# Kernel optimization log

Measured on AMD Instinct MI355X. Metric: run time of the kernel, lower is better.

The kernel has to match this reference:

```python
import jax, jax.numpy as jnp
import numpy as np

PIXEL_SIZE = 0.1
PI = 3.141592653589793


def setup_inputs() -> dict:
    key = jax.random.key(0)
    batch = jax.random.normal(key, (128, 1, 512, 512), dtype=jnp.float32)
    return {"batch": batch}


def _hann_window(roi):
    # lin = linspace(-roi/2, roi/2, roi); r[i,j] = sqrt(lin[j]^2 + lin[i]^2)
    lin = jnp.linspace(-roi / 2, roi / 2, roi, dtype=jnp.float32)
    r = jnp.sqrt(lin[None, :] ** 2 + lin[:, None] ** 2)
    hann = 0.5 * (1.0 + jnp.cos(PI * r / (roi / 2)))
    hann = jnp.where(r > roi / 2, 0.0, hann)
    return hann  # [roi, roi]


def _radial_segments(roi, n_freq):
    # radialDst = round(sqrt(xx^2 + yy^2)) with x = arange(-cx, roi-cx)
    cx = roi // 2
    x = np.arange(-cx, roi - cx, dtype=np.float64)
    xx, yy = np.meshgrid(x, x, indexing="ij")
    rad = np.round(np.sqrt(xx ** 2 + yy ** 2)).astype(np.int32)
    # bins >= n_freq go into an overflow segment that is discarded
    seg = np.where(rad < n_freq, rad, n_freq)
    return jnp.asarray(seg.ravel())


def reference(batch):
    px = PIXEL_SIZE
    roi = batch.shape[-1]
    cx = roi // 2
    n_freq = cx + 1
    nyquist = 1.0 / (2.0 * px)

    # subtract per-ROI mean
    batch_nm = batch - jnp.mean(batch, axis=(2, 3), keepdims=True)

    # Hann-windowed 2D power spectrum, averaged over realizations
    hann = _hann_window(roi)[None, None, :, :]
    F = jnp.fft.fftshift(jnp.fft.fft2(batch_nm * hann, axes=(2, 3)), axes=(2, 3))
    ps = jnp.mean(jnp.abs(F) ** 2, axis=0)            # [1, roi, roi]
    nps2D = (px ** 2 / roi ** 2) * jnp.squeeze(ps)    # [roi, roi]

    # single-pass radial mean binning (replaces per-k boolean-mask loop)
    seg = _radial_segments(roi, n_freq)
    flat = nps2D.ravel()
    sums = jax.ops.segment_sum(flat, seg, num_segments=n_freq + 1)[:n_freq]
    counts = jax.ops.segment_sum(jnp.ones_like(flat), seg, num_segments=n_freq + 1)[:n_freq]
    nps1D = sums / counts

    f1D = jnp.linspace(0.0, nyquist, n_freq, dtype=jnp.float32)
    return nps1D, nps2D, f1D
```

## Files before the change

kernel.cpp:

```cpp
#include <hip/hip_runtime.h>
#include <hip/hip_fp16.h>

#define N 512
#define NF 257
#define NB 128
#define PI_F 3.14159265358979323846f
#define C_SQ2 0.70710678118654752440f

__device__ __forceinline__ float2 cmul(float2 a, float2 b) {
    return make_float2(a.x * b.x - a.y * b.y, a.x * b.y + a.y * b.x);
}
__device__ __forceinline__ void bf(float2& a, float2& b) {
    float2 t = b;
    b = make_float2(a.x - t.x, a.y - t.y);
    a = make_float2(a.x + t.x, a.y + t.y);
}
__device__ __forceinline__ void bf_tw(float2& a, float2& b, float2 w) {
    float2 t = cmul(b, w);
    b = make_float2(a.x - t.x, a.y - t.y);
    a = make_float2(a.x + t.x, a.y + t.y);
}
__device__ __forceinline__ void bf_ni(float2& a, float2& b) {
    float2 t = make_float2(b.y, -b.x);
    b = make_float2(a.x - t.x, a.y - t.y);
    a = make_float2(a.x + t.x, a.y + t.y);
}
__device__ __forceinline__ void lds_order() {
    asm volatile("" ::: "memory");
}

__device__ __forceinline__ void fft_phaseA(float2 v[8]) {
    const float2 w64  = make_float2(C_SQ2, -C_SQ2);
    const float2 w192 = make_float2(-C_SQ2, -C_SQ2);
    bf(v[0], v[1]); bf(v[2], v[3]); bf(v[4], v[5]); bf(v[6], v[7]);
    bf(v[0], v[2]); bf_ni(v[1], v[3]); bf(v[4], v[6]); bf_ni(v[5], v[7]);
    bf(v[0], v[4]); bf_tw(v[1], v[5], w64); bf_ni(v[2], v[6]); bf_tw(v[3], v[7], w192);
}
__device__ __forceinline__ void fft_phaseBC(float2 v[8], float2 W1, float2 W1a,
                                            float2 W1n, float2 W1c, float2 W2,
                                            float2 W2n, float2 W3) {
    bf_tw(v[0], v[1], W3); bf_tw(v[2], v[3], W3); bf_tw(v[4], v[5], W3); bf_tw(v[6], v[7], W3);
    bf_tw(v[0], v[2], W2); bf_tw(v[1], v[3], W2n); bf_tw(v[4], v[6], W2); bf_tw(v[5], v[7], W2n);
    bf_tw(v[0], v[4], W1); bf_tw(v[1], v[5], W1a); bf_tw(v[2], v[6], W1n); bf_tw(v[3], v[7], W1c);
}

__device__ __forceinline__ void fft512_core(float2 v[8], float2* st, int l) {
    const float2 w64  = make_float2(C_SQ2, -C_SQ2);
    const float2 w192 = make_float2(-C_SQ2, -C_SQ2);
    int g = l >> 3, r = l & 7;
    lds_order();
    fft_phaseA(v);
#pragma unroll
    for (int e = 0; e < 8; e++) st[9 * l + e] = v[e];
    lds_order();
#pragma unroll
    for (int t = 0; t < 8; t++) v[t] = st[72 * g + 9 * t + r];
    float sn, cs;
    __sincosf(-(PI_F / 32.0f) * (float)r, &sn, &cs);
    float2 W1 = make_float2(cs, sn);
    float2 W2 = cmul(W1, W1);
    float2 W3 = cmul(W2, W2);
    float2 W2n = make_float2(W2.y, -W2.x);
    float2 W1a = cmul(W1, w64);
    float2 W1n = make_float2(W1.y, -W1.x);
    float2 W1c = cmul(W1, w192);
    fft_phaseBC(v, W1, W1a, W1n, W1c, W2, W2n, W3);
    lds_order();
#pragma unroll
    for (int t = 0; t < 8; t++) st[72 * g + 9 * t + r] = v[t];
    lds_order();
#pragma unroll
    for (int t = 0; t < 8; t++) v[t] = st[72 * t + l + (l >> 3)];
    __sincosf(-(PI_F / 256.0f) * (float)l, &sn, &cs);
    float2 Wc = make_float2(cs, sn);
    float2 w2 = cmul(Wc, Wc);
    float2 w4 = cmul(w2, w2);
    float2 w2n = make_float2(w2.y, -w2.x);
    float2 Wca = cmul(Wc, w64);
    float2 Wcn = make_float2(Wc.y, -Wc.x);
    float2 Wcc = cmul(Wc, w192);
    fft_phaseBC(v, Wc, Wca, Wcn, Wcc, w2, w2n, w4);
}

__device__ __forceinline__ void fft512_x2(float2 va[8], float2 vb[8], float2* st, int l) {
    const float2 w64  = make_float2(C_SQ2, -C_SQ2);
    const float2 w192 = make_float2(-C_SQ2, -C_SQ2);
    int g = l >> 3, r = l & 7;
    fft_phaseA(va); fft_phaseA(vb);
    lds_order();
#pragma unroll
    for (int e = 0; e < 8; e++) st[9 * l + e] = va[e];
    lds_order();
#pragma unroll
    for (int t = 0; t < 8; t++) va[t] = st[72 * g + 9 * t + r];
    lds_order();
#pragma unroll
    for (int e = 0; e < 8; e++) st[9 * l + e] = vb[e];
    lds_order();
#pragma unroll
    for (int t = 0; t < 8; t++) vb[t] = st[72 * g + 9 * t + r];
    float sn, cs;
    __sincosf(-(PI_F / 32.0f) * (float)r, &sn, &cs);
    float2 W1 = make_float2(cs, sn);
    float2 W2 = cmul(W1, W1);
    float2 W3 = cmul(W2, W2);
    float2 W2n = make_float2(W2.y, -W2.x);
    float2 W1a = cmul(W1, w64);
    float2 W1n = make_float2(W1.y, -W1.x);
    float2 W1c = cmul(W1, w192);
    fft_phaseBC(va, W1, W1a, W1n, W1c, W2, W2n, W3);
    fft_phaseBC(vb, W1, W1a, W1n, W1c, W2, W2n, W3);
    lds_order();
#pragma unroll
    for (int t = 0; t < 8; t++) st[72 * g + 9 * t + r] = va[t];
    lds_order();
#pragma unroll
    for (int t = 0; t < 8; t++) va[t] = st[72 * t + l + (l >> 3)];
    lds_order();
#pragma unroll
    for (int t = 0; t < 8; t++) st[72 * g + 9 * t + r] = vb[t];
    lds_order();
#pragma unroll
    for (int t = 0; t < 8; t++) vb[t] = st[72 * t + l + (l >> 3)];
    __sincosf(-(PI_F / 256.0f) * (float)l, &sn, &cs);
    float2 Wc = make_float2(cs, sn);
    float2 w2 = cmul(Wc, Wc);
    float2 w4 = cmul(w2, w2);
    float2 w2n = make_float2(w2.y, -w2.x);
    float2 Wca = cmul(Wc, w64);
    float2 Wcn = make_float2(Wc.y, -Wc.x);
    float2 Wcc = cmul(Wc, w192);
    fft_phaseBC(va, Wc, Wca, Wcn, Wcc, w2, w2n, w4);
    fft_phaseBC(vb, Wc, Wca, Wcn, Wcc, w2, w2n, w4);
}

__device__ __forceinline__ void unpack_rows(const float2 v[8], __half2* tile,
                                            int lr0, int lr1, int l, int sl) {
#pragma unroll
    for (int t = 0; t <= 4; t++) {
        float2 a = v[7 - t];
        float zfx = __shfl(a.x, sl);
        float zfy = __shfl(a.y, sl);
        if (l == 0) { float2 o = v[(8 - t) & 7]; zfx = o.x; zfy = o.y; }
        float2 z = v[t];
        int col = 64 * t + l;
        if (col < NF) {
            tile[lr0 * 265 + col] = __floats2half2_rn(0.5f * (z.x + zfx), 0.5f * (z.y - zfy));
            tile[lr1 * 265 + col] = __floats2half2_rn(0.5f * (z.y + zfy), 0.5f * (zfx - z.x));
        }
    }
}

__global__ void zero_kernel(float* __restrict__ accH, float* __restrict__ bins,
                            float* __restrict__ meanacc) {
    int i = blockIdx.x * blockDim.x + threadIdx.x;
    if (i < NF * N) accH[i] = 0.0f;
    if (i < 2 * (NF + 1)) bins[i] = 0.0f;
    if (i < NB) meanacc[i] = 0.0f;
}

__global__ __launch_bounds__(256) void hanntab_kernel(float* __restrict__ htab) {
    int i = blockIdx.x * 256 + threadIdx.x;
    int r = i >> 9, c = i & (N - 1);
    const float step = (float)N / (float)(N - 1);
    float a = -0.5f * (float)N + (float)r * step;
    float b = -0.5f * (float)N + (float)c * step;
    float rr = sqrtf(a * a + b * b);
    float h = (rr > 256.0f) ? 0.0f : 0.5f * (1.0f + cosf(rr * (PI_F / 256.0f)));
    htab[i] = h;
}

__global__ __launch_bounds__(512) void hannfft_kernel(const float* __restrict__ htab,
                                                      float2* __restrict__ Hrow) {
    __shared__ float sm[9216];
    int tid = threadIdx.x;
    int w = tid >> 6, l = tid & 63;
    int rowbase = blockIdx.x << 4;
    int r1 = rowbase + 2 * w;
    int rl = __brev((unsigned)l) >> 26;
    const int bre[8] = {0, 4, 2, 6, 1, 5, 3, 7};
    const float* h1 = htab + (size_t)r1 * N + rl;
    const float* h2 = h1 + N;

    float2 v[8];
#pragma unroll
    for (int e = 0; e < 8; e++) {
        int o = bre[e] << 6;
        v[e] = make_float2(h1[o], h2[o]);
    }

    float2* st = (float2*)sm + w * 576;
    fft512_core(v, st, l);
    __syncthreads();

    float* tre = sm;
    float* tim = sm + 4240;
    int lr0 = 2 * w, lr1 = lr0 + 1;
    int sl = (64 - l) & 63;
#pragma unroll
    for (int t = 0; t <= 4; t++) {
        float2 a = v[7 - t];
        float zfx = __shfl(a.x, sl);
        float zfy = __shfl(a.y, sl);
        if (l == 0) { float2 o = v[(8 - t) & 7]; zfx = o.x; zfy = o.y; }
        float2 z = v[t];
        int col = 64 * t + l;
        if (col < NF) {
            tre[lr0 * 265 + col] = 0.5f * (z.x + zfx);
            tim[lr0 * 265 + col] = 0.5f * (z.y - zfy);
            tre[lr1 * 265 + col] = 0.5f * (z.y + zfy);
            tim[lr1 * 265 + col] = 0.5f * (zfx - z.x);
        }
    }
    __syncthreads();

    int c0 = tid >> 4, rr = tid & 15;
#pragma unroll
    for (int it = 0; it < 9; it++) {
        int c = it * 32 + c0;
        if (c < NF) {
            float2 val = make_float2(tre[rr * 265 + c], tim[rr * 265 + c]);
            Hrow[(size_t)c * N + rowbase + rr] = val;
        }
    }
}

__global__ __launch_bounds__(512, 4) void rowfft_kernel(const float* __restrict__ x,
                                                        const float* __restrict__ htab,
                                                        float* __restrict__ meanacc,
                                                        __half2* __restrict__ inter) {
    __shared__ float sm[9216];
    __shared__ float redsum[8];
    int tid = threadIdx.x;
    int w = tid >> 6, l = tid & 63;
    int img = blockIdx.x >> 4;
    int rowbase = (blockIdx.x & 15) << 5;
    int r1 = rowbase + 4 * w;
    int rl = __brev((unsigned)l) >> 26;
    const int bre[8] = {0, 4, 2, 6, 1, 5, 3, 7};
    const float* xp = x + ((size_t)img * N + r1) * N + rl;
    const float* hp = htab + (size_t)r1 * N + rl;

    float ax[4][8], hx[4][8];
#pragma unroll
    for (int j = 0; j < 4; j++)
#pragma unroll
        for (int e = 0; e < 8; e++) ax[j][e] = xp[j * N + (bre[e] << 6)];
#pragma unroll
    for (int j = 0; j < 4; j++)
#pragma unroll
        for (int e = 0; e < 8; e++) hx[j][e] = hp[j * N + (bre[e] << 6)];
    __builtin_amdgcn_sched_barrier(0);

    float rsum = 0.0f;
#pragma unroll
    for (int j = 0; j < 4; j++)
#pragma unroll
        for (int e = 0; e < 8; e++) rsum += ax[j][e];

    float2 va[8], vb[8];
#pragma unroll
    for (int e = 0; e < 8; e++) {
        va[e] = make_float2(ax[0][e] * hx[0][e], ax[1][e] * hx[1][e]);
        vb[e] = make_float2(ax[2][e] * hx[2][e], ax[3][e] * hx[3][e]);
    }

#pragma unroll
    for (int off = 32; off > 0; off >>= 1) rsum += __shfl_down(rsum, off);
    if (l == 0) redsum[w] = rsum;

    float2* st = (float2*)sm + w * 576;
    fft512_x2(va, vb, st, l);
    __syncthreads();
    if (tid == 0) {
        float s = 0.0f;
#pragma unroll
        for (int i = 0; i < 8; i++) s += redsum[i];
        atomicAdd(meanacc + img, s);
    }

    __half2* tile = (__half2*)sm;
    int sl = (64 - l) & 63;
    unpack_rows(va, tile, 4 * w, 4 * w + 1, l, sl);
    unpack_rows(vb, tile, 4 * w + 2, 4 * w + 3, l, sl);
    __syncthreads();

    int c0 = tid >> 5, rr = tid & 31;
#pragma unroll
    for (int it = 0; it < 17; it++) {
        int c = it * 16 + c0;
        if (c < NF) {
            inter[((size_t)img * NF + c) * N + rowbase + rr] = tile[rr * 265 + c];
        }
    }
}

__global__ __launch_bounds__(256, 4) void colfft_kernel(const __half2* __restrict__ inter,
                                                        const float2* __restrict__ Hrow,
                                                        const float* __restrict__ meanacc,
                                                        float* __restrict__ accH) {
    __shared__ float sm[4608];
    int tid = threadIdx.x;
    int w = tid >> 6, l = tid & 63;
    int col = blockIdx.x * 4 + w;
    int colc = col < NF ? col : NF - 1;
    int b0 = blockIdx.y * 4;
    float2* st = (float2*)sm + w * 576;
    int rl = __brev((unsigned)l) >> 26;
    const int bre[8] = {0, 4, 2, 6, 1, 5, 3, 7};

    float2 hc[8];
    const float2* hp = Hrow + (size_t)colc * N + rl;
#pragma unroll
    for (int e = 0; e < 8; e++) hc[e] = hp[bre[e] << 6];

    float mn[4];
#pragma unroll
    for (int i = 0; i < 4; i++)
        mn[i] = meanacc[b0 + i] * (1.0f / ((float)N * (float)N));

    float pw[8];
#pragma unroll
    for (int t = 0; t < 8; t++) pw[t] = 0.0f;

    const size_t istr = (size_t)NF * N;
    const __half2* base = inter + ((size_t)b0 * NF + colc) * N + rl;

    __half2 cA[8], cB[8], nA[8], nB[8];
#pragma unroll
    for (int e = 0; e < 8; e++) {
        cA[e] = base[bre[e] << 6];
        cB[e] = base[istr + (bre[e] << 6)];
    }
    __builtin_amdgcn_sched_barrier(0);

#pragma unroll
    for (int it = 0; it < 2; it++) {
        if (it == 0) {
#pragma unroll
            for (int e = 0; e < 8; e++) {
                nA[e] = base[2 * istr + (bre[e] << 6)];
                nB[e] = base[3 * istr + (bre[e] << 6)];
            }
        }
        float mA = mn[2 * it], mB = mn[2 * it + 1];
        float2 va[8], vb[8];
#pragma unroll
        for (int e = 0; e < 8; e++) {
            float2 zA = __half22float2(cA[e]);
            float2 zB = __half22float2(cB[e]);
            va[e] = make_float2(zA.x - mA * hc[e].x, zA.y - mA * hc[e].y);
            vb[e] = make_float2(zB.x - mB * hc[e].x, zB.y - mB * hc[e].y);
        }
        fft512_x2(va, vb, st, l);
#pragma unroll
        for (int t = 0; t < 8; t++)
            pw[t] += va[t].x * va[t].x + va[t].y * va[t].y
                   + vb[t].x * vb[t].x + vb[t].y * vb[t].y;
#pragma unroll
        for (int e = 0; e < 8; e++) { cA[e] = nA[e]; cB[e] = nB[e]; }
    }

    if (col < NF) {
#pragma unroll
        for (int t = 0; t < 8; t++)
            atomicAdd(&accH[(size_t)col * N + 64 * t + l], pw[t]);
    }
}

__global__ __launch_bounds__(256) void finalize2d_kernel(const float* __restrict__ accH,
                                                         float* __restrict__ out2d,
                                                         float* __restrict__ bins) {
    __shared__ float lsum[NF];
    __shared__ float lcnt[NF];
    int t = threadIdx.x;
    for (int i = t; i < NF; i += 256) { lsum[i] = 0.0f; lcnt[i] = 0.0f; }
    __syncthreads();
    const float scale = (0.1f * 0.1f) / ((float)N * (float)N) / (float)NB;
    int idx = blockIdx.x * 256 + t;
    int stride = gridDim.x * 256;
    for (int p = idx; p < N * N; p += stride) {
        int i = p >> 9, j = p & (N - 1);
        int jm = (j + 256) & 511;
        int col, k;
        if (jm < NF) { col = jm; k = (i + 256) & 511; }
        else         { col = 256 - j; k = (256 - i) & 511; }
        float v = accH[((size_t)col << 9) + k] * scale;
        out2d[p] = v;
        float xi = (float)(i - 256), yj = (float)(j - 256);
        int rad = (int)rintf(sqrtf(xi * xi + yj * yj));
        if (rad < NF) { atomicAdd(&lsum[rad], v); atomicAdd(&lcnt[rad], 1.0f); }
    }
    __syncthreads();
    for (int i = t; i < NF; i += 256) {
        if (lsum[i] != 0.0f || lcnt[i] != 0.0f) {
            atomicAdd(&bins[i], lsum[i]);
            atomicAdd(&bins[NF + 1 + i], lcnt[i]);
        }
    }
}

__global__ void finalize1d_kernel(const float* __restrict__ bins, float* __restrict__ out) {
    int t = blockIdx.x * blockDim.x + threadIdx.x;
    if (t < NF) {
        out[t] = bins[t] / bins[NF + 1 + t];
        out[NF + N * N + t] = (float)t * (5.0f / 256.0f);
    }
}

extern "C" void kernel_launch(void* const* d_in, const int* in_sizes, int n_in,
                              void* d_out, int out_size, void* d_ws, size_t ws_size,
                              hipStream_t stream) {
    const float* x = (const float*)d_in[0];
    float* out = (float*)d_out;
    char* ws = (char*)d_ws;

    float* accH    = (float*)ws;
    float* meanacc = (float*)(ws + (size_t)NF * N * sizeof(float));
    float* bins    = meanacc + NB;
    size_t off_h = (size_t)NF * N * sizeof(float) + NB * sizeof(float)
                   + 2 * (NF + 1) * sizeof(float);
    off_h = (off_h + 255) & ~(size_t)255;
    float2* Hrow = (float2*)(ws + off_h);
    size_t off_t = off_h + (size_t)NF * N * sizeof(float2);
    off_t = (off_t + 255) & ~(size_t)255;
    float* htab = (float*)(ws + off_t);
    size_t off_inter = off_t + (size_t)N * N * sizeof(float);
    off_inter = (off_inter + 255) & ~(size_t)255;
    __half2* inter = (__half2*)(ws + off_inter);

    zero_kernel<<<dim3((NF * N + 255) / 256), dim3(256), 0, stream>>>(accH, bins, meanacc);
    hanntab_kernel<<<dim3(N * N / 256), dim3(256), 0, stream>>>(htab);
    hannfft_kernel<<<dim3(32), dim3(512), 0, stream>>>(htab, Hrow);
    rowfft_kernel<<<dim3(NB * 16), dim3(512), 0, stream>>>(x, htab, meanacc, inter);
    colfft_kernel<<<dim3(65, 32), dim3(256), 0, stream>>>(inter, Hrow, meanacc, accH);
    finalize2d_kernel<<<dim3(256), dim3(256), 0, stream>>>(accH, out + NF, bins);
    finalize1d_kernel<<<dim3(2), dim3(256), 0, stream>>>(bins, out);
}
```

Baseline: 256.1 us.

## Fold Hann-FFT and zeroing into other kernels and shrink row-FFT blocks

Merges the zero kernel into the Hann-table kernel and moves the Hann-window row FFT into extra blocks of the row-FFT kernel, which removes two launches. The row-FFT blocks shrink from 512 to 256 threads (16 rows per block, 8 blocks per CU hint) and twice as many blocks are launched. The sched_barrier is dropped and finalize2d gets more blocks. The Hann blocks now write Hrow directly with strided stores instead of staging through LDS, and they share the grid with the image row-FFT blocks.

Result: slower. 295.9 us (+15.5%).

```diff
diff --git a/kernel.cpp b/kernel.cpp
--- a/kernel.cpp
+++ b/kernel.cpp
@@ -42,44 +42,6 @@
     bf_tw(v[0], v[1], W3); bf_tw(v[2], v[3], W3); bf_tw(v[4], v[5], W3); bf_tw(v[6], v[7], W3);
     bf_tw(v[0], v[2], W2); bf_tw(v[1], v[3], W2n); bf_tw(v[4], v[6], W2); bf_tw(v[5], v[7], W2n);
     bf_tw(v[0], v[4], W1); bf_tw(v[1], v[5], W1a); bf_tw(v[2], v[6], W1n); bf_tw(v[3], v[7], W1c);
-}
-
-__device__ __forceinline__ void fft512_core(float2 v[8], float2* st, int l) {
-    const float2 w64  = make_float2(C_SQ2, -C_SQ2);
-    const float2 w192 = make_float2(-C_SQ2, -C_SQ2);
-    int g = l >> 3, r = l & 7;
-    lds_order();
-    fft_phaseA(v);
-#pragma unroll
-    for (int e = 0; e < 8; e++) st[9 * l + e] = v[e];
-    lds_order();
-#pragma unroll
-    for (int t = 0; t < 8; t++) v[t] = st[72 * g + 9 * t + r];
-    float sn, cs;
-    __sincosf(-(PI_F / 32.0f) * (float)r, &sn, &cs);
-    float2 W1 = make_float2(cs, sn);
-    float2 W2 = cmul(W1, W1);
-    float2 W3 = cmul(W2, W2);
-    float2 W2n = make_float2(W2.y, -W2.x);
-    float2 W1a = cmul(W1, w64);
-    float2 W1n = make_float2(W1.y, -W1.x);
-    float2 W1c = cmul(W1, w192);
-    fft_phaseBC(v, W1, W1a, W1n, W1c, W2, W2n, W3);
-    lds_order();
-#pragma unroll
-    for (int t = 0; t < 8; t++) st[72 * g + 9 * t + r] = v[t];
-    lds_order();
-#pragma unroll
-    for (int t = 0; t < 8; t++) v[t] = st[72 * t + l + (l >> 3)];
-    __sincosf(-(PI_F / 256.0f) * (float)l, &sn, &cs);
-    float2 Wc = make_float2(cs, sn);
-    float2 w2 = cmul(Wc, Wc);
-    float2 w4 = cmul(w2, w2);
-    float2 w2n = make_float2(w2.y, -w2.x);
-    float2 Wca = cmul(Wc, w64);
-    float2 Wcn = make_float2(Wc.y, -Wc.x);
-    float2 Wcc = cmul(Wc, w192);
-    fft_phaseBC(v, Wc, Wca, Wcn, Wcc, w2, w2n, w4);
 }
 
 __device__ __forceinline__ void fft512_x2(float2 va[8], float2 vb[8], float2* st, int l) {
@@ -151,15 +113,27 @@
     }
 }
 
-__global__ void zero_kernel(float* __restrict__ accH, float* __restrict__ bins,
-                            float* __restrict__ meanacc) {
-    int i = blockIdx.x * blockDim.x + threadIdx.x;
-    if (i < NF * N) accH[i] = 0.0f;
-    if (i < 2 * (NF + 1)) bins[i] = 0.0f;
-    if (i < NB) meanacc[i] = 0.0f;
-}
-
-__global__ __launch_bounds__(256) void hanntab_kernel(float* __restrict__ htab) {
+__device__ __forceinline__ void unpack_rows_store(const float2 v[8], float2* __restrict__ Hrow,
+                                                  int r0, int r1, int l, int sl) {
+#pragma unroll
+    for (int t = 0; t <= 4; t++) {
+        float2 a = v[7 - t];
+        float zfx = __shfl(a.x, sl);
+        float zfy = __shfl(a.y, sl);
+        if (l == 0) { float2 o = v[(8 - t) & 7]; zfx = o.x; zfy = o.y; }
+        float2 z = v[t];
+        int col = 64 * t + l;
+        if (col < NF) {
+            Hrow[(size_t)col * N + r0] = make_float2(0.5f * (z.x + zfx), 0.5f * (z.y - zfy));
+            Hrow[(size_t)col * N + r1] = make_float2(0.5f * (z.y + zfy), 0.5f * (zfx - z.x));
+        }
+    }
+}
+
+__global__ __launch_bounds__(256) void hanntab_zero_kernel(float* __restrict__ htab,
+                                                           float* __restrict__ accH,
+                                                           float* __restrict__ bins,
+                                                           float* __restrict__ meanacc) {
     int i = blockIdx.x * 256 + threadIdx.x;
     int r = i >> 9, c = i & (N - 1);
     const float step = (float)N / (float)(N - 1);
@@ -168,76 +142,49 @@
     float rr = sqrtf(a * a + b * b);
     float h = (rr > 256.0f) ? 0.0f : 0.5f * (1.0f + cosf(rr * (PI_F / 256.0f)));
     htab[i] = h;
-}
-
-__global__ __launch_bounds__(512) void hannfft_kernel(const float* __restrict__ htab,
-                                                      float2* __restrict__ Hrow) {
-    __shared__ float sm[9216];
+    if (i < NF * N) accH[i] = 0.0f;
+    if (i < 2 * (NF + 1)) bins[i] = 0.0f;
+    if (i < NB) meanacc[i] = 0.0f;
+}
+
+__global__ __launch_bounds__(256, 8) void rowfft_kernel(const float* __restrict__ x,
+                                                        const float* __restrict__ htab,
+                                                        float* __restrict__ meanacc,
+                                                        __half2* __restrict__ inter,
+                                                        float2* __restrict__ Hrow) {
+    __shared__ __align__(16) float sm[4608];
+    __shared__ float redsum[4];
     int tid = threadIdx.x;
     int w = tid >> 6, l = tid & 63;
-    int rowbase = blockIdx.x << 4;
-    int r1 = rowbase + 2 * w;
     int rl = __brev((unsigned)l) >> 26;
     const int bre[8] = {0, 4, 2, 6, 1, 5, 3, 7};
-    const float* h1 = htab + (size_t)r1 * N + rl;
-    const float* h2 = h1 + N;
-
-    float2 v[8];
-#pragma unroll
-    for (int e = 0; e < 8; e++) {
-        int o = bre[e] << 6;
-        v[e] = make_float2(h1[o], h2[o]);
-    }
-
     float2* st = (float2*)sm + w * 576;
-    fft512_core(v, st, l);
-    __syncthreads();
-
-    float* tre = sm;
-    float* tim = sm + 4240;
-    int lr0 = 2 * w, lr1 = lr0 + 1;
     int sl = (64 - l) & 63;
-#pragma unroll
-    for (int t = 0; t <= 4; t++) {
-        float2 a = v[7 - t];
-        float zfx = __shfl(a.x, sl);
-        float zfy = __shfl(a.y, sl);
-        if (l == 0) { float2 o = v[(8 - t) & 7]; zfx = o.x; zfy = o.y; }
-        float2 z = v[t];
-        int col = 64 * t + l;
-        if (col < NF) {
-            tre[lr0 * 265 + col] = 0.5f * (z.x + zfx);
-            tim[lr0 * 265 + col] = 0.5f * (z.y - zfy);
-            tre[lr1 * 265 + col] = 0.5f * (z.y + zfy);
-            tim[lr1 * 265 + col] = 0.5f * (zfx - z.x);
-        }
-    }
-    __syncthreads();
-
-    int c0 = tid >> 4, rr = tid & 15;
-#pragma unroll
-    for (int it = 0; it < 9; it++) {
-        int c = it * 32 + c0;
-        if (c < NF) {
-            float2 val = make_float2(tre[rr * 265 + c], tim[rr * 265 + c]);
-            Hrow[(size_t)c * N + rowbase + rr] = val;
-        }
-    }
-}
-
-__global__ __launch_bounds__(512, 4) void rowfft_kernel(const float* __restrict__ x,
-                                                        const float* __restrict__ htab,
-                                                        float* __restrict__ meanacc,
-                                                        __half2* __restrict__ inter) {
-    __shared__ float sm[9216];
-    __shared__ float redsum[8];
-    int tid = threadIdx.x;
-    int w = tid >> 6, l = tid & 63;
-    int img = blockIdx.x >> 4;
-    int rowbase = (blockIdx.x & 15) << 5;
+
+    if (blockIdx.x >= NB * 32) {
+        int hb = blockIdx.x - NB * 32;
+        int r1 = (hb << 4) + 4 * w;
+        const float* hp = htab + (size_t)r1 * N + rl;
+        float hx[4][8];
+#pragma unroll
+        for (int j = 0; j < 4; j++)
+#pragma unroll
+            for (int e = 0; e < 8; e++) hx[j][e] = hp[j * N + (bre[e] << 6)];
+        float2 va[8], vb[8];
+#pragma unroll
+        for (int e = 0; e < 8; e++) {
+            va[e] = make_float2(hx[0][e], hx[1][e]);
+            vb[e] = make_float2(hx[2][e], hx[3][e]);
+        }
+        fft512_x2(va, vb, st, l);
+        unpack_rows_store(va, Hrow, r1, r1 + 1, l, sl);
+        unpack_rows_store(vb, Hrow, r1 + 2, r1 + 3, l, sl);
+        return;
+    }
+
+    int img = blockIdx.x >> 5;
+    int rowbase = (blockIdx.x & 31) << 4;
     int r1 = rowbase + 4 * w;
-    int rl = __brev((unsigned)l) >> 26;
-    const int bre[8] = {0, 4, 2, 6, 1, 5, 3, 7};
     const float* xp = x + ((size_t)img * N + r1) * N + rl;
     const float* hp = htab + (size_t)r1 * N + rl;
 
@@ -250,7 +197,6 @@
     for (int j = 0; j < 4; j++)
 #pragma unroll
         for (int e = 0; e < 8; e++) hx[j][e] = hp[j * N + (bre[e] << 6)];
-    __builtin_amdgcn_sched_barrier(0);
 
     float rsum = 0.0f;
 #pragma unroll
@@ -269,23 +215,21 @@
     for (int off = 32; off > 0; off >>= 1) rsum += __shfl_down(rsum, off);
     if (l == 0) redsum[w] = rsum;
 
-    float2* st = (float2*)sm + w * 576;
     fft512_x2(va, vb, st, l);
     __syncthreads();
     if (tid == 0) {
         float s = 0.0f;
 #pragma unroll
-        for (int i = 0; i < 8; i++) s += redsum[i];
+        for (int i = 0; i < 4; i++) s += redsum[i];
         atomicAdd(meanacc + img, s);
     }
 
     __half2* tile = (__half2*)sm;
-    int sl = (64 - l) & 63;
     unpack_rows(va, tile, 4 * w, 4 * w + 1, l, sl);
     unpack_rows(vb, tile, 4 * w + 2, 4 * w + 3, l, sl);
     __syncthreads();
 
-    int c0 = tid >> 5, rr = tid & 31;
+    int c0 = tid >> 4, rr = tid & 15;
 #pragma unroll
     for (int it = 0; it < 17; it++) {
         int c = it * 16 + c0;
@@ -299,7 +243,7 @@
                                                         const float2* __restrict__ Hrow,
                                                         const float* __restrict__ meanacc,
                                                         float* __restrict__ accH) {
-    __shared__ float sm[4608];
+    __shared__ __align__(16) float sm[4608];
     int tid = threadIdx.x;
     int w = tid >> 6, l = tid & 63;
     int col = blockIdx.x * 4 + w;
@@ -429,11 +373,9 @@
     off_inter = (off_inter + 255) & ~(size_t)255;
     __half2* inter = (__half2*)(ws + off_inter);
 
-    zero_kernel<<<dim3((NF * N + 255) / 256), dim3(256), 0, stream>>>(accH, bins, meanacc);
-    hanntab_kernel<<<dim3(N * N / 256), dim3(256), 0, stream>>>(htab);
-    hannfft_kernel<<<dim3(32), dim3(512), 0, stream>>>(htab, Hrow);
-    rowfft_kernel<<<dim3(NB * 16), dim3(512), 0, stream>>>(x, htab, meanacc, inter);
+    hanntab_zero_kernel<<<dim3(N * N / 256), dim3(256), 0, stream>>>(htab, accH, bins, meanacc);
+    rowfft_kernel<<<dim3(NB * 32 + 32), dim3(256), 0, stream>>>(x, htab, meanacc, inter, Hrow);
     colfft_kernel<<<dim3(65, 32), dim3(256), 0, stream>>>(inter, Hrow, meanacc, accH);
-    finalize2d_kernel<<<dim3(256), dim3(256), 0, stream>>>(accH, out + NF, bins);
+    finalize2d_kernel<<<dim3(512), dim3(256), 0, stream>>>(accH, out + NF, bins);
     finalize1d_kernel<<<dim3(2), dim3(256), 0, stream>>>(bins, out);
 }
```
